# Performance work log

Hardware: AMD Instinct MI355X
Metric: run time of the kernel (lower is better)

## Reference

```python
import jax, jax.numpy as jnp
import numpy as np

SCALE, K_UP = 2, 5
EPS = 1e-5  # nn.BatchNorm2d default


def _bn(x, g, b, m, v):
    # inference batchnorm over channel axis 1
    inv = g / jnp.sqrt(v + EPS)
    return x * inv[None, :, None, None] + (b - m * inv)[None, :, None, None]


def _conv(x, w, pad):
    return jax.lax.conv_general_dilated(
        x, w, (1, 1), [(pad, pad), (pad, pad)],
        dimension_numbers=('NCHW', 'OIHW', 'NCHW'))


def setup_inputs() -> dict:
    key = jax.random.key(0)
    ks = jax.random.split(key, 12)
    b, c, h, w = 16, 256, 80, 80
    c_mid, k2s2 = 64, (SCALE * K_UP) ** 2  # 100
    return {
        'X': jax.random.normal(ks[0], (b, c, h, w), jnp.float32),
        'w_comp': jax.random.normal(ks[1], (c_mid, c, 1, 1), jnp.float32) * 0.05,
        'g1': jax.random.uniform(ks[2], (c_mid,), jnp.float32, 0.5, 1.5),
        'b1': jax.random.normal(ks[3], (c_mid,), jnp.float32) * 0.05,
        'm1': jax.random.normal(ks[4], (c_mid,), jnp.float32) * 0.05,
        'v1': jax.random.uniform(ks[5], (c_mid,), jnp.float32, 0.5, 1.5),
        'w_enc': jax.random.normal(ks[6], (k2s2, c_mid, 3, 3), jnp.float32) * 0.05,
        'g2': jax.random.uniform(ks[7], (k2s2,), jnp.float32, 0.5, 1.5),
        'b2': jax.random.normal(ks[8], (k2s2,), jnp.float32) * 0.05,
        'm2': jax.random.normal(ks[9], (k2s2,), jnp.float32) * 0.05,
        'v2': jax.random.uniform(ks[10], (k2s2,), jnp.float32, 0.5, 1.5),
    }


def reference(X, w_comp, g1, b1, m1, v1, w_enc, g2, b2, m2, v2):
    b, c, h, w = X.shape
    s, k = SCALE, K_UP
    h_, w_ = h * s, w * s
    k2 = k * k
    # comp: 1x1 conv + BN + SiLU
    Wm = jax.nn.silu(_bn(_conv(X, w_comp, 0), g1, b1, m1, v1))
    # enc: 3x3 conv + BN, no activation -> (b, (s*k)^2, h, w)
    Wm = _bn(_conv(Wm, w_enc, 1), g2, b2, m2, v2)
    # PixelShuffle(s): (b, s*s*k2, h, w) -> (b, k2, h*s, w*s)
    Wm = Wm.reshape(b, k2, s, s, h, w).transpose(0, 1, 4, 2, 5, 3).reshape(b, k2, h_, w_)
    Wm = jax.nn.softmax(Wm, axis=1)
    # nearest upsample of X by s
    Xup = jnp.repeat(jnp.repeat(X, s, axis=2), s, axis=3)
    # unfold(kernel=k, dilation=s, padding=k//2*s) + weighted sum, computed
    # as 25 shifted slices (row-major kernel index ki*k+kj matches unfold)
    pad = (k // 2) * s
    Xp = jnp.pad(Xup, ((0, 0), (0, 0), (pad, pad), (pad, pad)))
    out = jnp.zeros((b, c, h_, w_), X.dtype)
    for ki in range(k):
        for kj in range(k):
            patch = jax.lax.dynamic_slice(Xp, (0, 0, ki * s, kj * s), (b, c, h_, w_))
            out = out + Wm[:, ki * k + kj][:, None] * patch
    return out
```

## Files before the change

### kernel.cpp

```cpp
#include <hip/hip_runtime.h>
#include <hip/hip_bf16.h>


#define NB   16
#define CIN  256
#define HH   80
#define WW   80
#define HWP  6400
#define CMID 64
#define OH   160
#define OW   160
#define OHW  25600

__global__ __launch_bounds__(256) void k1_conv1x1(
    const float* __restrict__ X, const float* __restrict__ Wc,
    const float* __restrict__ g1, const float* __restrict__ b1,
    const float* __restrict__ m1, const float* __restrict__ v1,
    float* __restrict__ Y) {
  __shared__ float wlds[128 * 64];
  const int tid = threadIdx.x;
  const int p = blockIdx.x * 256 + tid;
  const int b = p / HWP;
  const int hw = p - b * HWP;
  const float* Xb = X + (size_t)b * CIN * HWP + hw;

  float acc[64];
#pragma unroll
  for (int i = 0; i < 64; ++i) acc[i] = 0.f;

  for (int half = 0; half < 2; ++half) {
    __syncthreads();
    for (int i = tid; i < 128 * 64; i += 256) {
      int cl = i >> 6, oc = i & 63;
      wlds[i] = Wc[(size_t)oc * CIN + half * 128 + cl];
    }
    __syncthreads();
#pragma unroll 4
    for (int cl = 0; cl < 128; ++cl) {
      float xv = Xb[(size_t)(half * 128 + cl) * HWP];
      const float4* wr = (const float4*)&wlds[cl * 64];
#pragma unroll
      for (int j = 0; j < 16; ++j) {
        float4 wv = wr[j];
        acc[j * 4 + 0] += wv.x * xv;
        acc[j * 4 + 1] += wv.y * xv;
        acc[j * 4 + 2] += wv.z * xv;
        acc[j * 4 + 3] += wv.w * xv;
      }
    }
  }

  float* Yb = Y + (size_t)b * CMID * HWP + hw;
#pragma unroll
  for (int oc = 0; oc < 64; ++oc) {
    float inv = g1[oc] * rsqrtf(v1[oc] + 1e-5f);
    float v = acc[oc] * inv + (b1[oc] - m1[oc] * inv);
    Yb[(size_t)oc * HWP] = v / (1.f + __expf(-v));
  }
}

__global__ __launch_bounds__(320) void k2_conv3x3_softmax(
    const float* __restrict__ Y, const float* __restrict__ We,
    const float* __restrict__ g2, const float* __restrict__ b2,
    const float* __restrict__ m2, const float* __restrict__ v2,
    float* __restrict__ Wsm) {
  __shared__ float wlds[576 * 28];
  const int tid = threadIdx.x;
  const int b = blockIdx.y;
  const int off = blockIdx.z;
  const int si = off >> 1, sj = off & 1;

  for (int i = tid; i < 576 * 25; i += 320) {
    int k576 = i / 25, q = i - k576 * 25;
    int ch = q * 4 + off;
    float inv = g2[ch] * rsqrtf(v2[ch] + 1e-5f);
    wlds[k576 * 28 + q] = We[(size_t)ch * 576 + k576] * inv;
  }
  __syncthreads();

  const int p0 = blockIdx.x * 640 + tid;
  const int p1 = p0 + 320;
  const int h0 = p0 / 80, w0 = p0 - h0 * 80;
  const int h1 = p1 / 80, w1 = p1 - h1 * 80;
  const float* Yb = Y + (size_t)b * CMID * HWP;

  float acc0[25], acc1[25];
#pragma unroll
  for (int q = 0; q < 25; ++q) { acc0[q] = 0.f; acc1[q] = 0.f; }

  bool rv0[3], cv0[3], rv1[3], cv1[3];
  int ro0[3], co0[3], ro1[3], co1[3];
#pragma unroll
  for (int d = 0; d < 3; ++d) {
    int r0 = h0 + d - 1, c0 = w0 + d - 1, r1 = h1 + d - 1, c1 = w1 + d - 1;
    rv0[d] = (r0 >= 0 && r0 < 80); ro0[d] = r0 * 80;
    cv0[d] = (c0 >= 0 && c0 < 80); co0[d] = c0;
    rv1[d] = (r1 >= 0 && r1 < 80); ro1[d] = r1 * 80;
    cv1[d] = (c1 >= 0 && c1 < 80); co1[d] = c1;
  }

  for (int c = 0; c < 64; ++c) {
    float ya[9], yb[9];
    const float* Yc = Yb + (size_t)c * HWP;
#pragma unroll
    for (int dh = 0; dh < 3; ++dh)
#pragma unroll
      for (int dw = 0; dw < 3; ++dw) {
        ya[dh * 3 + dw] = (rv0[dh] && cv0[dw]) ? Yc[ro0[dh] + co0[dw]] : 0.f;
        yb[dh * 3 + dw] = (rv1[dh] && cv1[dw]) ? Yc[ro1[dh] + co1[dw]] : 0.f;
      }
#pragma unroll
    for (int k = 0; k < 9; ++k) {
      const float4* wr = (const float4*)&wlds[(c * 9 + k) * 28];
      float xa = ya[k], xb = yb[k];
#pragma unroll
      for (int j = 0; j < 6; ++j) {
        float4 wv = wr[j];
        acc0[j * 4 + 0] += wv.x * xa; acc1[j * 4 + 0] += wv.x * xb;
        acc0[j * 4 + 1] += wv.y * xa; acc1[j * 4 + 1] += wv.y * xb;
        acc0[j * 4 + 2] += wv.z * xa; acc1[j * 4 + 2] += wv.z * xb;
        acc0[j * 4 + 3] += wv.w * xa; acc1[j * 4 + 3] += wv.w * xb;
      }
      float wl = wlds[(c * 9 + k) * 28 + 24];
      acc0[24] += wl * xa; acc1[24] += wl * xb;
    }
  }

#pragma unroll 1
  for (int px = 0; px < 2; ++px) {
    float* a = px ? acc1 : acc0;
    int h = px ? h1 : h0, w = px ? w1 : w0;
    float mx = -3.4e38f;
#pragma unroll
    for (int q = 0; q < 25; ++q) {
      int ch = q * 4 + off;
      float inv = g2[ch] * rsqrtf(v2[ch] + 1e-5f);
      a[q] += b2[ch] - m2[ch] * inv;
      mx = fmaxf(mx, a[q]);
    }
    float s = 0.f;
#pragma unroll
    for (int q = 0; q < 25; ++q) { a[q] = __expf(a[q] - mx); s += a[q]; }
    float rs = 1.f / s;
    size_t base = (size_t)b * 25 * OHW + (size_t)(2 * h + si) * OW + (2 * w + sj);
#pragma unroll
    for (int q = 0; q < 25; ++q) Wsm[base + (size_t)q * OHW] = a[q] * rs;
  }
}

__global__ __launch_bounds__(256) void k3_carafe(
    const float* __restrict__ X, const float* __restrict__ Wsm,
    float* __restrict__ Out) {
  __shared__ float wlds[1600];
  __shared__ float xlds[32 * 105];

  const int tid = threadIdx.x;
  const int wt = blockIdx.x;
  const int h = blockIdx.y;
  const int b = blockIdx.z;
  const int wl = tid & 15, ci = tid >> 4;

  for (int i = tid; i < 1600; i += 256) {
    int wli = i & 15;
    int r = i >> 4;
    int t = r % 25, ss = r / 25;
    int sy = ss >> 1, sx = ss & 1;
    wlds[i] = Wsm[(size_t)(b * 25 + t) * OHW + (size_t)(2 * h + sy) * OW +
                  wt * 32 + 2 * wli + sx];
  }
  __syncthreads();

  float wr[100];
#pragma unroll
  for (int r = 0; r < 100; ++r) wr[r] = wlds[r * 16 + wl];

  const float* Xb = X + (size_t)b * CIN * HWP;

  for (int cc = 0; cc < 8; ++cc) {
    __syncthreads();
    for (int i = tid; i < 3200; i += 256) {
      int cl = i / 100;
      int rem = i - cl * 100;
      int di = rem / 20, j = rem - di * 20;
      int r = h + di - 2;
      int col = wt * 16 + j - 2;
      float v = 0.f;
      if (r >= 0 && r < 80 && col >= 0 && col < 80)
        v = Xb[(size_t)(cc * 32 + cl) * HWP + r * 80 + col];
      xlds[cl * 105 + di * 21 + j] = v;
    }
    __syncthreads();
#pragma unroll
    for (int half = 0; half < 2; ++half) {
      int cl = ci + half * 16;
      int c = cc * 32 + cl;
      float xp[25];
#pragma unroll
      for (int t = 0; t < 25; ++t)
        xp[t] = xlds[cl * 105 + (t / 5) * 21 + wl + (t % 5)];
      float a00 = 0.f, a01 = 0.f, a10 = 0.f, a11 = 0.f;
#pragma unroll
      for (int t = 0; t < 25; ++t) {
        a00 += wr[t] * xp[t];
        a01 += wr[25 + t] * xp[t];
        a10 += wr[50 + t] * xp[t];
        a11 += wr[75 + t] * xp[t];
      }
      size_t ob = (size_t)(b * 256 + c) * OHW + (size_t)(2 * h) * OW +
                  wt * 32 + 2 * wl;
      *(float2*)&Out[ob] = make_float2(a00, a01);
      *(float2*)&Out[ob + OW] = make_float2(a10, a11);
    }
  }
}

extern "C" void kernel_launch(void* const* d_in, const int* in_sizes, int n_in,
                              void* d_out, int out_size, void* d_ws, size_t ws_size,
                              hipStream_t stream) {
  const float* X  = (const float*)d_in[0];
  const float* Wc = (const float*)d_in[1];
  const float* g1 = (const float*)d_in[2];
  const float* b1 = (const float*)d_in[3];
  const float* m1 = (const float*)d_in[4];
  const float* v1 = (const float*)d_in[5];
  const float* We = (const float*)d_in[6];
  const float* g2 = (const float*)d_in[7];
  const float* b2 = (const float*)d_in[8];
  const float* m2 = (const float*)d_in[9];
  const float* v2 = (const float*)d_in[10];
  float* Out = (float*)d_out;

  float* Y   = (float*)d_ws;
  float* Wsm = (float*)((char*)d_ws + (size_t)26214400);

  k1_conv1x1<<<400, 256, 0, stream>>>(X, Wc, g1, b1, m1, v1, Y);
  k2_conv3x3_softmax<<<dim3(10, 16, 4), 320, 0, stream>>>(Y, We, g2, b2, m2, v2, Wsm);
  k3_carafe<<<dim3(5, 80, 16), 256, 0, stream>>>(X, Wsm, Out);
}
```

Before: 1.506 ms.

## Tile conv3x3 through LDS, change Wsm layout, double-buffer CARAFE with swizzled grid

```diff
diff --git a/kernel.cpp b/kernel.cpp
--- a/kernel.cpp
+++ b/kernel.cpp
@@ -2,14 +2,7 @@
 #include <hip/hip_bf16.h>
 
 
-#define NB   16
-#define CIN  256
-#define HH   80
-#define WW   80
 #define HWP  6400
-#define CMID 64
-#define OH   160
-#define OW   160
 #define OHW  25600
 
 __global__ __launch_bounds__(256) void k1_conv1x1(
@@ -22,7 +15,7 @@
   const int p = blockIdx.x * 256 + tid;
   const int b = p / HWP;
   const int hw = p - b * HWP;
-  const float* Xb = X + (size_t)b * CIN * HWP + hw;
+  const float* Xb = X + (size_t)b * 256 * HWP + hw;
 
   float acc[64];
 #pragma unroll
@@ -32,7 +25,7 @@
     __syncthreads();
     for (int i = tid; i < 128 * 64; i += 256) {
       int cl = i >> 6, oc = i & 63;
-      wlds[i] = Wc[(size_t)oc * CIN + half * 128 + cl];
+      wlds[i] = Wc[(size_t)oc * 256 + half * 128 + cl];
     }
     __syncthreads();
 #pragma unroll 4
@@ -50,7 +43,7 @@
     }
   }
 
-  float* Yb = Y + (size_t)b * CMID * HWP + hw;
+  float* Yb = Y + (size_t)b * 64 * HWP + hw;
 #pragma unroll
   for (int oc = 0; oc < 64; ++oc) {
     float inv = g1[oc] * rsqrtf(v1[oc] + 1e-5f);
@@ -64,72 +57,92 @@
     const float* __restrict__ g2, const float* __restrict__ b2,
     const float* __restrict__ m2, const float* __restrict__ v2,
     float* __restrict__ Wsm) {
-  __shared__ float wlds[576 * 28];
+  __shared__ float ylds[6400];
+  __shared__ float wlds[72 * 28];
   const int tid = threadIdx.x;
+  const int bx = blockIdx.x;
   const int b = blockIdx.y;
   const int off = blockIdx.z;
-  const int si = off >> 1, sj = off & 1;
-
-  for (int i = tid; i < 576 * 25; i += 320) {
-    int k576 = i / 25, q = i - k576 * 25;
-    int ch = q * 4 + off;
-    float inv = g2[ch] * rsqrtf(v2[ch] + 1e-5f);
-    wlds[k576 * 28 + q] = We[(size_t)ch * 576 + k576] * inv;
-  }
-  __syncthreads();
-
-  const int p0 = blockIdx.x * 640 + tid;
+  const int h0 = bx * 8;
+
+  const int p0 = bx * 640 + tid;
   const int p1 = p0 + 320;
-  const int h0 = p0 / 80, w0 = p0 - h0 * 80;
-  const int h1 = p1 / 80, w1 = p1 - h1 * 80;
-  const float* Yb = Y + (size_t)b * CMID * HWP;
+  const int h0p = p0 / 80, w0 = p0 - h0p * 80;
+  const int h1p = p1 / 80, w1 = p1 - h1p * 80;
+  const int lr0 = h0p - h0, lr1 = h1p - h0;
+
+  int gy[20];
+  unsigned ymask = 0;
+#pragma unroll
+  for (int k = 0; k < 20; ++k) {
+    int i = k * 320 + tid;
+    int cl = (unsigned)i / 800u;
+    int rem = i - cl * 800;
+    int r = (unsigned)rem / 80u;
+    int col = rem - r * 80;
+    int grow = h0 - 1 + r;
+    gy[k] = ((b * 64 + cl) * 80 + grow) * 80 + col;
+    if (grow >= 0 && grow < 80) ymask |= (1u << k);
+  }
 
   float acc0[25], acc1[25];
 #pragma unroll
   for (int q = 0; q < 25; ++q) { acc0[q] = 0.f; acc1[q] = 0.f; }
 
-  bool rv0[3], cv0[3], rv1[3], cv1[3];
-  int ro0[3], co0[3], ro1[3], co1[3];
+  bool cv0[3], cv1[3];
+  int co0[3], co1[3];
 #pragma unroll
   for (int d = 0; d < 3; ++d) {
-    int r0 = h0 + d - 1, c0 = w0 + d - 1, r1 = h1 + d - 1, c1 = w1 + d - 1;
-    rv0[d] = (r0 >= 0 && r0 < 80); ro0[d] = r0 * 80;
+    int c0 = w0 - 1 + d, c1 = w1 - 1 + d;
     cv0[d] = (c0 >= 0 && c0 < 80); co0[d] = c0;
-    rv1[d] = (r1 >= 0 && r1 < 80); ro1[d] = r1 * 80;
     cv1[d] = (c1 >= 0 && c1 < 80); co1[d] = c1;
   }
 
-  for (int c = 0; c < 64; ++c) {
-    float ya[9], yb[9];
-    const float* Yc = Yb + (size_t)c * HWP;
-#pragma unroll
-    for (int dh = 0; dh < 3; ++dh)
-#pragma unroll
-      for (int dw = 0; dw < 3; ++dw) {
-        ya[dh * 3 + dw] = (rv0[dh] && cv0[dw]) ? Yc[ro0[dh] + co0[dw]] : 0.f;
-        yb[dh * 3 + dw] = (rv1[dh] && cv1[dw]) ? Yc[ro1[dh] + co1[dw]] : 0.f;
-      }
-#pragma unroll
-    for (int k = 0; k < 9; ++k) {
-      const float4* wr = (const float4*)&wlds[(c * 9 + k) * 28];
-      float xa = ya[k], xb = yb[k];
-#pragma unroll
-      for (int j = 0; j < 6; ++j) {
-        float4 wv = wr[j];
-        acc0[j * 4 + 0] += wv.x * xa; acc1[j * 4 + 0] += wv.x * xb;
-        acc0[j * 4 + 1] += wv.y * xa; acc1[j * 4 + 1] += wv.y * xb;
-        acc0[j * 4 + 2] += wv.z * xa; acc1[j * 4 + 2] += wv.z * xb;
-        acc0[j * 4 + 3] += wv.w * xa; acc1[j * 4 + 3] += wv.w * xb;
-      }
-      float wl = wlds[(c * 9 + k) * 28 + 24];
-      acc0[24] += wl * xa; acc1[24] += wl * xb;
-    }
-  }
-
-#pragma unroll 1
-  for (int px = 0; px < 2; ++px) {
-    float* a = px ? acc1 : acc0;
-    int h = px ? h1 : h0, w = px ? w1 : w0;
+  for (int cc = 0; cc < 8; ++cc) {
+    __syncthreads();
+#pragma unroll
+    for (int k = 0; k < 20; ++k) {
+      float v = 0.f;
+      if (ymask & (1u << k)) v = Y[gy[k] + cc * 8 * HWP];
+      ylds[k * 320 + tid] = v;
+    }
+    for (int i = tid; i < 1800; i += 320) {
+      int rw = (unsigned)i / 25u, q = i - rw * 25;
+      int ch = q * 4 + off;
+      float inv = g2[ch] * rsqrtf(v2[ch] + 1e-5f);
+      wlds[rw * 28 + q] = We[(size_t)ch * 576 + cc * 72 + rw] * inv;
+    }
+    __syncthreads();
+
+    for (int c8 = 0; c8 < 8; ++c8) {
+      float ya[9], yb[9];
+      const float* yc = &ylds[c8 * 800];
+#pragma unroll
+      for (int dh = 0; dh < 3; ++dh)
+#pragma unroll
+        for (int dw = 0; dw < 3; ++dw) {
+          ya[dh * 3 + dw] = cv0[dw] ? yc[(lr0 + dh) * 80 + co0[dw]] : 0.f;
+          yb[dh * 3 + dw] = cv1[dw] ? yc[(lr1 + dh) * 80 + co1[dw]] : 0.f;
+        }
+#pragma unroll
+      for (int k = 0; k < 9; ++k) {
+        const float4* wrp = (const float4*)&wlds[(c8 * 9 + k) * 28];
+        float xa = ya[k], xb = yb[k];
+#pragma unroll
+        for (int j = 0; j < 6; ++j) {
+          float4 wv = wrp[j];
+          acc0[j * 4 + 0] += wv.x * xa; acc1[j * 4 + 0] += wv.x * xb;
+          acc0[j * 4 + 1] += wv.y * xa; acc1[j * 4 + 1] += wv.y * xb;
+          acc0[j * 4 + 2] += wv.z * xa; acc1[j * 4 + 2] += wv.z * xb;
+          acc0[j * 4 + 3] += wv.w * xa; acc1[j * 4 + 3] += wv.w * xb;
+        }
+        float wl = wlds[(c8 * 9 + k) * 28 + 24];
+        acc0[24] += wl * xa; acc1[24] += wl * xb;
+      }
+    }
+  }
+
+  auto epi = [&](float (&a)[25], int h, int w) {
     float mx = -3.4e38f;
 #pragma unroll
     for (int q = 0; q < 25; ++q) {
@@ -142,75 +155,104 @@
 #pragma unroll
     for (int q = 0; q < 25; ++q) { a[q] = __expf(a[q] - mx); s += a[q]; }
     float rs = 1.f / s;
-    size_t base = (size_t)b * 25 * OHW + (size_t)(2 * h + si) * OW + (2 * w + sj);
-#pragma unroll
-    for (int q = 0; q < 25; ++q) Wsm[base + (size_t)q * OHW] = a[q] * rs;
-  }
-}
-
-__global__ __launch_bounds__(256) void k3_carafe(
+    size_t base = ((size_t)(b * 25) * 4 + off) * HWP + h * 80 + w;
+#pragma unroll
+    for (int q = 0; q < 25; ++q) Wsm[base + (size_t)q * 4 * HWP] = a[q] * rs;
+  };
+  epi(acc0, h0p, w0);
+  epi(acc1, h1p, w1);
+}
+
+#define XDIM 1920
+
+__global__ __launch_bounds__(256, 3) void k3_carafe(
     const float* __restrict__ X, const float* __restrict__ Wsm,
     float* __restrict__ Out) {
-  __shared__ float wlds[1600];
-  __shared__ float xlds[32 * 105];
-
+  __shared__ float lds[3840];
   const int tid = threadIdx.x;
-  const int wt = blockIdx.x;
-  const int h = blockIdx.y;
-  const int b = blockIdx.z;
+  const int bid = blockIdx.x;
+  const int swz = (bid & 7) * 800 + (bid >> 3);
+  const int wt = swz % 5;
+  const int h = (swz / 5) % 80;
+  const int b = swz / 400;
   const int wl = tid & 15, ci = tid >> 4;
 
   for (int i = tid; i < 1600; i += 256) {
-    int wli = i & 15;
-    int r = i >> 4;
+    int wli = i & 15, r = i >> 4;
     int t = r % 25, ss = r / 25;
-    int sy = ss >> 1, sx = ss & 1;
-    wlds[i] = Wsm[(size_t)(b * 25 + t) * OHW + (size_t)(2 * h + sy) * OW +
-                  wt * 32 + 2 * wli + sx];
+    lds[i] = Wsm[(size_t)((b * 25 + t) * 4 + ss) * HWP + h * 80 + wt * 16 + wli];
   }
   __syncthreads();
-
   float wr[100];
 #pragma unroll
-  for (int r = 0; r < 100; ++r) wr[r] = wlds[r * 16 + wl];
-
-  const float* Xb = X + (size_t)b * CIN * HWP;
-
-  for (int cc = 0; cc < 8; ++cc) {
-    __syncthreads();
-    for (int i = tid; i < 3200; i += 256) {
-      int cl = i / 100;
-      int rem = i - cl * 100;
-      int di = rem / 20, j = rem - di * 20;
-      int r = h + di - 2;
-      int col = wt * 16 + j - 2;
-      float v = 0.f;
-      if (r >= 0 && r < 80 && col >= 0 && col < 80)
-        v = Xb[(size_t)(cc * 32 + cl) * HWP + r * 80 + col];
-      xlds[cl * 105 + di * 21 + j] = v;
-    }
-    __syncthreads();
-#pragma unroll
-    for (int half = 0; half < 2; ++half) {
-      int cl = ci + half * 16;
-      int c = cc * 32 + cl;
-      float xp[25];
-#pragma unroll
-      for (int t = 0; t < 25; ++t)
-        xp[t] = xlds[cl * 105 + (t / 5) * 21 + wl + (t % 5)];
-      float a00 = 0.f, a01 = 0.f, a10 = 0.f, a11 = 0.f;
-#pragma unroll
-      for (int t = 0; t < 25; ++t) {
-        a00 += wr[t] * xp[t];
-        a01 += wr[25 + t] * xp[t];
-        a10 += wr[50 + t] * xp[t];
-        a11 += wr[75 + t] * xp[t];
-      }
-      size_t ob = (size_t)(b * 256 + c) * OHW + (size_t)(2 * h) * OW +
-                  wt * 32 + 2 * wl;
-      *(float2*)&Out[ob] = make_float2(a00, a01);
-      *(float2*)&Out[ob + OW] = make_float2(a10, a11);
-    }
+  for (int r = 0; r < 100; ++r) wr[r] = lds[r * 16 + wl];
+  __syncthreads();
+
+  int gofs[8];
+  unsigned vmask = 0;
+#pragma unroll
+  for (int k = 0; k < 8; ++k) {
+    int i = k * 256 + tid;
+    int cl = (unsigned)i / 120u;
+    int rem = i - cl * 120;
+    int di = (unsigned)rem / 24u;
+    int j = rem - di * 24;
+    int row = h + di - 2;
+    int col = wt * 16 + j - 2;
+    bool ok = (i < XDIM) && (j < 20) && row >= 0 && row < 80 && col >= 0 && col < 80;
+    gofs[k] = ((b * 256 + cl) * 80 + row) * 80 + col;
+    if (ok) vmask |= (1u << k);
+  }
+
+#pragma unroll
+  for (int k = 0; k < 8; ++k) {
+    int i = k * 256 + tid;
+    float v = 0.f;
+    if (vmask & (1u << k)) v = X[gofs[k]];
+    if (i < XDIM) lds[i] = v;
+  }
+  __syncthreads();
+
+  const int xbase = ci * 120 + wl;
+  size_t obase = ((size_t)(b * 256 + ci) * 160 + 2 * h) * 160 + wt * 32 + 2 * wl;
+
+#pragma unroll 2
+  for (int cc = 0; cc < 16; ++cc) {
+    const int cur = (cc & 1) * XDIM;
+    const int nxt = XDIM - cur;
+
+    float pv[8];
+    if (cc < 15) {
+#pragma unroll
+      for (int k = 0; k < 8; ++k) {
+        pv[k] = 0.f;
+        if (vmask & (1u << k)) pv[k] = X[gofs[k] + (cc + 1) * 16 * HWP];
+      }
+    }
+
+    const float* xb = &lds[cur + xbase];
+    float a00 = 0.f, a01 = 0.f, a10 = 0.f, a11 = 0.f;
+#pragma unroll
+    for (int t = 0; t < 25; ++t) {
+      float xv = xb[(t / 5) * 24 + (t % 5)];
+      a00 += wr[t] * xv;
+      a01 += wr[25 + t] * xv;
+      a10 += wr[50 + t] * xv;
+      a11 += wr[75 + t] * xv;
+    }
+
+    if (cc < 15) {
+#pragma unroll
+      for (int k = 0; k < 8; ++k) {
+        int i = k * 256 + tid;
+        if (i < XDIM) lds[nxt + i] = pv[k];
+      }
+    }
+
+    float* op = Out + obase + (size_t)cc * 16 * OHW;
+    *(float2*)op = make_float2(a00, a01);
+    *(float2*)(op + 160) = make_float2(a10, a11);
+    __syncthreads();
   }
 }
 
@@ -235,5 +277,5 @@
 
   k1_conv1x1<<<400, 256, 0, stream>>>(X, Wc, g1, b1, m1, v1, Y);
   k2_conv3x3_softmax<<<dim3(10, 16, 4), 320, 0, stream>>>(Y, We, g2, b2, m2, v2, Wsm);
-  k3_carafe<<<dim3(5, 80, 16), 256, 0, stream>>>(X, Wsm, Out);
-}
+  k3_carafe<<<dim3(6400), 256, 0, stream>>>(X, Wsm, Out);
+}
```

After: 1.314 ms. 1.15x faster.
